# Performance work log

Hardware: AMD Instinct MI355X
Metric: run time of the kernel (lower is better)

Reference implementation:

```python
import jax, jax.numpy as jnp
import numpy as np
from math import log

B, L, D = 2, 4096, 2048
H, Dh, C, KW = 16, 128, 64, 4
EPS = 1e-5
SCALE = 0.02


def setup_inputs() -> dict:
    key = jax.random.key(0)
    ks = jax.random.split(key, 16)
    rn = lambda k, shp, sc=SCALE: jax.random.normal(k, shp, jnp.float32) * sc
    # dt_bias built like the torch module
    dt = jnp.exp(jax.random.uniform(ks[7], (H,)) * (log(0.1) - log(0.001)) + log(0.001))
    dt = jnp.clip(dt, 0.0001, None)
    dt_bias = dt + jnp.log(-jnp.expm1(-dt))
    return {
        "x": jax.random.normal(ks[0], (B, L, D), jnp.float32),
        "Wq": rn(ks[1], (H * Dh, D)),
        "Wk": rn(ks[2], (H * Dh, D)),
        "Wv": rn(ks[3], (H * Dh, D)),
        "Wb": rn(ks[4], (H, D)),
        "Wa": rn(ks[5], (H, D)),
        "A_log": jnp.log(jax.random.uniform(ks[6], (H,), minval=0.01, maxval=16.0)),
        "dt_bias": dt_bias,
        "conv_q": rn(ks[8], (H * Dh, 1, KW), 0.2),
        "conv_k": rn(ks[9], (H * Dh, 1, KW), 0.2),
        "conv_v": rn(ks[10], (H * Dh, 1, KW), 0.2),
        "Wg": rn(ks[11], (H * Dh, D)),
        "norm_w": jnp.ones((Dh,), jnp.float32),
        "Wo": rn(ks[12], (D, H * Dh)),
        "S0": jnp.zeros((B, H, Dh, Dh), jnp.float32),
    }


def _causal_dwconv(x, w):
    # x: [B,L,Ch]; w: [Ch,1,KW] depthwise causal conv (left pad KW-1), then SiLU
    y = jax.lax.conv_general_dilated(
        x.transpose(0, 2, 1), w, (1,), [(KW - 1, 0)],
        feature_group_count=w.shape[0], dimension_numbers=("NCH", "OIH", "NCH"))
    return jax.nn.silu(y).transpose(0, 2, 1)


def reference(x, Wq, Wk, Wv, Wb, Wa, A_log, dt_bias, conv_q, conv_k, conv_v, Wg, norm_w, Wo, S0):
    q = _causal_dwconv(x @ Wq.T, conv_q).reshape(B, L, H, Dh).transpose(0, 2, 1, 3)  # [B,H,L,Dh]
    k = _causal_dwconv(x @ Wk.T, conv_k).reshape(B, L, H, Dh).transpose(0, 2, 1, 3)
    v = _causal_dwconv(x @ Wv.T, conv_v).reshape(B, L, H, Dh).transpose(0, 2, 1, 3)
    beta = jax.nn.sigmoid(x @ Wb.T).transpose(0, 2, 1)                                # [B,H,L]
    g = (-jnp.exp(A_log) * jax.nn.softplus(x @ Wa.T + dt_bias)).transpose(0, 2, 1)    # [B,H,L]
    l2 = lambda t: t / jnp.maximum(jnp.linalg.norm(t, axis=-1, keepdims=True), 1e-12)
    q = l2(q) / (Dh ** 0.5)
    k = l2(k)

    N = L // C  # chunks (L divisible by C)
    chop = lambda t: jnp.moveaxis(t.reshape(B, H, N, C, Dh), 2, 0)   # [N,B,H,C,Dh]
    qc, kc, vc = chop(q), chop(k), chop(v)
    betac = jnp.moveaxis(beta.reshape(B, H, N, C), 2, 0)[..., None]  # [N,B,H,C,1]
    gc = jnp.moveaxis(g.reshape(B, H, N, C), 2, 0)                   # [N,B,H,C]

    eye = jnp.eye(C, dtype=x.dtype)
    m_incl = jnp.tril(jnp.ones((C, C), bool))
    m_strict = jnp.tril(jnp.ones((C, C), bool), -1)

    def step(S, ch):
        Q, Kc, V, bet, gch = ch
        lg = jnp.cumsum(gch, axis=-1)          # log gamma, [B,H,C]
        gamma = jnp.exp(lg)
        lgC = lg[..., -1:]
        gCr = jnp.exp(lgC - lg)
        gammaC = jnp.exp(lgC)[..., None]       # [B,H,1,1]
        Qd = Q * gamma[..., None]
        Kd = gCr[..., None] * Kc
        Sd = S * gammaC
        Gam = lg[..., :, None] - lg[..., None, :]
        ratio = jnp.exp(jnp.where(m_strict, Gam, -jnp.inf))
        A = eye + bet * ratio * (Kc @ jnp.swapaxes(Kc, -1, -2))
        T = jax.scipy.linalg.solve_triangular(A, jnp.broadcast_to(eye, A.shape), lower=True)
        Wm = T @ (bet * gamma[..., None] * Kc)
        U = T @ (bet * V)
        St = jnp.swapaxes(S, -1, -2)
        GM = jnp.exp(jnp.where(m_incl, Gam, -jnp.inf))
        mid = U - Wm @ St                      # [B,H,C,Dh]
        O = Qd @ St + ((Q @ jnp.swapaxes(Kc, -1, -2)) * GM) @ mid
        S_new = Sd + jnp.swapaxes(mid, -1, -2) @ Kd
        return S_new, O

    S_fin, Os = jax.lax.scan(step, S0, (qc, kc, vc, betac, gc))
    o = Os.transpose(1, 0, 3, 2, 4).reshape(B, L, H, Dh)  # chunks -> [B,L,H,Dh]
    gate = (x @ Wg.T).reshape(B, L, H, Dh)
    # gated RMSNorm: rms-normalize o, scale by weight, gate with SiLU(g)
    o = o * jax.lax.rsqrt(jnp.mean(o * o, axis=-1, keepdims=True) + EPS) * norm_w * jax.nn.silu(gate)
    return (o.reshape(B, L, H * Dh) @ Wo.T, S_fin)
```

## Files before the change

kernel.cpp:

```cpp
#include <hip/hip_runtime.h>
#include <math.h>

#define B_   2
#define L_   4096
#define D_   2048
#define H_   16
#define DH   128
#define CH   64
#define NCH  64
#define HD   2048
#define BH   32
#define BHL  131072
#define PSZ  16777216ull

typedef unsigned short u16;
typedef __attribute__((ext_vector_type(8))) short bf16x8;
typedef __attribute__((ext_vector_type(4))) float f32x4;
#define MFMA16(a, b, c) __builtin_amdgcn_mfma_f32_16x16x32_bf16(a, b, c, 0, 0, 0)

static __device__ __forceinline__ float sigm(float x) { return 1.0f / (1.0f + expf(-x)); }

static __device__ __forceinline__ float b2f(u16 u) {
    union { float f; unsigned int i; } v; v.i = ((unsigned int)u) << 16; return v.f;
}
static __device__ __forceinline__ u16 f2b(float f) {
    union { float f; unsigned int i; } v; v.f = f;
    unsigned int r = v.i + 0x7fffu + ((v.i >> 16) & 1u);
    return (u16)(r >> 16);
}
static __device__ __forceinline__ void b8ld(const u16* p, float* d) {
    uint4 u = *(const uint4*)p;
    d[0] = b2f((u16)(u.x & 0xffff)); d[1] = b2f((u16)(u.x >> 16));
    d[2] = b2f((u16)(u.y & 0xffff)); d[3] = b2f((u16)(u.y >> 16));
    d[4] = b2f((u16)(u.z & 0xffff)); d[5] = b2f((u16)(u.z >> 16));
    d[6] = b2f((u16)(u.w & 0xffff)); d[7] = b2f((u16)(u.w >> 16));
}
static __device__ __forceinline__ void b8st(const float* s, u16* p) {
    uint4 u;
    u.x = (unsigned)f2b(s[0]) | ((unsigned)f2b(s[1]) << 16);
    u.y = (unsigned)f2b(s[2]) | ((unsigned)f2b(s[3]) << 16);
    u.z = (unsigned)f2b(s[4]) | ((unsigned)f2b(s[5]) << 16);
    u.w = (unsigned)f2b(s[6]) | ((unsigned)f2b(s[7]) << 16);
    *(uint4*)p = u;
}
static __device__ __forceinline__ void cstore(float* p, float v) { *p = v; }
static __device__ __forceinline__ void cstore(u16* p, float v) { *p = f2b(v); }

static __device__ __forceinline__ void async16(const u16* g, u16* l) {
    __builtin_amdgcn_global_load_lds(
        (const __attribute__((address_space(1))) unsigned int*)g,
        (__attribute__((address_space(3))) unsigned int*)l, 16, 0, 0);
}

static __device__ __forceinline__ void bar_lgkm() {
    asm volatile("s_waitcnt lgkmcnt(0)" ::: "memory");
    __builtin_amdgcn_sched_barrier(0);
    __builtin_amdgcn_s_barrier();
    __builtin_amdgcn_sched_barrier(0);
}
static __device__ __forceinline__ void wait_vm0() {
    asm volatile("s_waitcnt vmcnt(0)" ::: "memory");
    __builtin_amdgcn_sched_barrier(0);
}

__global__ __launch_bounds__(256) void cvt_f2b(const float* __restrict__ in,
                                               u16* __restrict__ out, int n8) {
    int i = blockIdx.x * 256 + threadIdx.x;
    if (i >= n8) return;
    float t[8];
    float4 a = *(const float4*)(in + (size_t)i * 8);
    float4 b = *(const float4*)(in + (size_t)i * 8 + 4);
    t[0] = a.x; t[1] = a.y; t[2] = a.z; t[3] = a.w;
    t[4] = b.x; t[5] = b.y; t[6] = b.z; t[7] = b.w;
    b8st(t, out + (size_t)i * 8);
}

template <typename TC>
__global__ __launch_bounds__(256) void gemm_bt_async(const u16* __restrict__ A,
                                                     const u16* __restrict__ Bm,
                                                     TC* __restrict__ Cm,
                                                     int M, int N, int K) {
    __shared__ __align__(16) u16 sA[128 * 64];
    __shared__ __align__(16) u16 sB[128 * 64];
    const int tid = threadIdx.x;
    const int w = tid >> 6, lane = tid & 63, lq = lane >> 4, ln = lane & 15;
    const int wm = w >> 1, wn = w & 1;
    const int mbase = blockIdx.y * 128, nbase = blockIdx.x * 128;

    f32x4 acc[4][4];
#pragma unroll
    for (int mt = 0; mt < 4; mt++)
#pragma unroll
        for (int nt = 0; nt < 4; nt++) acc[mt][nt] = (f32x4){0.f, 0.f, 0.f, 0.f};

    for (int k0 = 0; k0 < K; k0 += 64) {
#pragma unroll
        for (int j = 0; j < 4; j++) {
            int c = tid + 256 * j;
            int row = c >> 3;
            int oct = (c & 7) ^ (row & 7);
            async16(A + (size_t)(mbase + row) * K + k0 + oct * 8, &sA[c * 8]);
            async16(Bm + (size_t)(nbase + row) * K + k0 + oct * 8, &sB[c * 8]);
        }
        __syncthreads();
#pragma unroll
        for (int ks = 0; ks < 2; ks++) {
            const int o = ks * 4 + lq;
            bf16x8 af[4], bfr[4];
#pragma unroll
            for (int mt = 0; mt < 4; mt++) {
                int m = wm * 64 + mt * 16 + ln;
                af[mt] = *(const bf16x8*)&sA[(m << 6) + ((o ^ (m & 7)) << 3)];
            }
#pragma unroll
            for (int nt = 0; nt < 4; nt++) {
                int nn = wn * 64 + nt * 16 + ln;
                bfr[nt] = *(const bf16x8*)&sB[(nn << 6) + ((o ^ (nn & 7)) << 3)];
            }
#pragma unroll
            for (int mt = 0; mt < 4; mt++)
#pragma unroll
                for (int nt = 0; nt < 4; nt++)
                    acc[mt][nt] = MFMA16(af[mt], bfr[nt], acc[mt][nt]);
        }
        __syncthreads();
    }
#pragma unroll
    for (int mt = 0; mt < 4; mt++)
#pragma unroll
        for (int nt = 0; nt < 4; nt++) {
            int col = nbase + wn * 64 + nt * 16 + ln;
#pragma unroll
            for (int r = 0; r < 4; r++) {
                int row = mbase + wm * 64 + mt * 16 + lq * 4 + r;
                cstore(Cm + (size_t)row * N + col, acc[mt][nt][r]);
            }
        }
}

__global__ __launch_bounds__(256) void conv_silu_norm(const u16* __restrict__ pre,
                                                      const float* __restrict__ w,
                                                      u16* __restrict__ out, int mode) {
    int wid = blockIdx.x * 4 + (threadIdx.x >> 6);
    int lane = threadIdx.x & 63;
    int l = wid & (L_ - 1);
    int bh = wid >> 12;
    int b = bh >> 4, h = bh & 15;

    float vals[2];
    float sumsq = 0.0f;
#pragma unroll
    for (int s = 0; s < 2; s++) {
        int d = lane + 64 * s;
        int c = h * DH + d;
        const u16* col = pre + (size_t)b * L_ * HD + c;
        float acc = 0.0f;
        if (l >= 3) {
            acc = w[c * 4 + 0] * b2f(col[(size_t)(l - 3) * HD]) +
                  w[c * 4 + 1] * b2f(col[(size_t)(l - 2) * HD]) +
                  w[c * 4 + 2] * b2f(col[(size_t)(l - 1) * HD]) +
                  w[c * 4 + 3] * b2f(col[(size_t)l * HD]);
        } else {
#pragma unroll
            for (int j = 0; j < 4; j++) {
                int ll = l - 3 + j;
                if (ll >= 0) acc += w[c * 4 + j] * b2f(col[(size_t)ll * HD]);
            }
        }
        float y = acc * sigm(acc);
        vals[s] = y;
        sumsq += y * y;
    }
    if (mode < 2) {
#pragma unroll
        for (int m = 32; m >= 1; m >>= 1) sumsq += __shfl_xor(sumsq, m, 64);
        float scale = 1.0f / fmaxf(sqrtf(sumsq), 1e-12f);
        if (mode == 0) scale *= 0.08838834764831843f;
        vals[0] *= scale;
        vals[1] *= scale;
    }
    u16* o = out + ((size_t)bh * L_ + l) * DH;
    o[lane] = f2b(vals[0]);
    o[lane + 64] = f2b(vals[1]);
}

__global__ __launch_bounds__(64) void proj_small(const float* __restrict__ x,
                                                 const float* __restrict__ Wb,
                                                 const float* __restrict__ Wa,
                                                 float* __restrict__ bpre,
                                                 float* __restrict__ apre) {
    int row = blockIdx.x;
    int lane = threadIdx.x;
    const float* xr = x + (size_t)row * D_;
    float xv[32];
#pragma unroll
    for (int j = 0; j < 32; j++) xv[j] = xr[lane + 64 * j];
    for (int h = 0; h < 16; h++) {
        const float* wr = Wb + (size_t)h * D_;
        float acc = 0.0f;
#pragma unroll
        for (int j = 0; j < 32; j++) acc += xv[j] * wr[lane + 64 * j];
#pragma unroll
        for (int m = 32; m >= 1; m >>= 1) acc += __shfl_xor(acc, m, 64);
        if (lane == 0) bpre[(size_t)row * 16 + h] = acc;
    }
    for (int h = 0; h < 16; h++) {
        const float* wr = Wa + (size_t)h * D_;
        float acc = 0.0f;
#pragma unroll
        for (int j = 0; j < 32; j++) acc += xv[j] * wr[lane + 64 * j];
#pragma unroll
        for (int m = 32; m >= 1; m >>= 1) acc += __shfl_xor(acc, m, 64);
        if (lane == 0) apre[(size_t)row * 16 + h] = acc;
    }
}

__global__ __launch_bounds__(256) void beta_g_k(const float* __restrict__ bpre,
                                                const float* __restrict__ apre,
                                                const float* __restrict__ A_log,
                                                const float* __restrict__ dt_bias,
                                                float* __restrict__ beta, float* __restrict__ g) {
    int gi = blockIdx.x * 256 + threadIdx.x;
    int l = gi & (L_ - 1);
    int bh = gi >> 12;
    int b = bh >> 4, h = bh & 15;
    float bp = bpre[((size_t)b * L_ + l) * 16 + h];
    float ap = apre[((size_t)b * L_ + l) * 16 + h] + dt_bias[h];
    float sp = (ap > 20.0f) ? ap : log1pf(expf(ap));
    beta[(size_t)bh * L_ + l] = 1.0f / (1.0f + expf(-bp));
    g[(size_t)bh * L_ + l] = -expf(A_log[h]) * sp;
}

__global__ __launch_bounds__(256) void prep_chunks(u16* __restrict__ q, u16* __restrict__ k,
                                                   u16* __restrict__ v,
                                                   const float* __restrict__ beta,
                                                   const float* __restrict__ g,
                                                   u16* __restrict__ Wm, u16* __restrict__ W2,
                                                   float* __restrict__ gamC) {
    __shared__ __align__(16) u16 sKb[64 * 136];
    __shared__ __align__(16) float sA[64 * 65];
    __shared__ __align__(16) float sT[64 * 68];
    __shared__ float sLg[CH], sGam[CH], sGcr[CH], sBeta[CH];

    const int cid = blockIdx.x;
    const int bh = cid >> 6, n = cid & 63;
    const int tid = threadIdx.x;
    const int w = tid >> 6, lane = tid & 63, lq = lane >> 4, ln = lane & 15;
    const size_t cbase = ((size_t)bh * L_ + (size_t)n * CH) * DH;
    u16* qw = q + cbase;
    u16* kw = k + cbase;
    u16* vc = v + cbase;

    bf16x8 aQ[4];
    {
        const u16* qrow = qw + (size_t)(w * 16 + ln) * DH;
#pragma unroll
        for (int ks = 0; ks < 4; ks++)
            aQ[ks] = *(const bf16x8*)(qrow + ks * 32 + lq * 8);
    }
#pragma unroll
    for (int rep = 0; rep < 4; rep++) {
        int f = tid + 256 * rep;
        int row = f >> 4, c8 = (f & 15) * 8;
        *(uint4*)&sKb[row * 136 + c8] = *(const uint4*)(kw + (size_t)row * DH + c8);
    }
    if (tid < 64) {
        float lg = g[(size_t)bh * L_ + (size_t)n * CH + tid];
#pragma unroll
        for (int off = 1; off < 64; off <<= 1) {
            float u = __shfl_up(lg, off, 64);
            if (tid >= off) lg += u;
        }
        float lgC = __shfl(lg, 63, 64);
        sLg[tid] = lg;
        sGam[tid] = expf(lg);
        sGcr[tid] = expf(lgC - lg);
        sBeta[tid] = beta[(size_t)bh * L_ + (size_t)n * CH + tid];
        if (tid == 63) gamC[cid] = expf(lgC);
    }
    __syncthreads();

    {
        f32x4 accA[4], accQ[4];
#pragma unroll
        for (int nt = 0; nt < 4; nt++) {
            accA[nt] = (f32x4){0.f, 0.f, 0.f, 0.f};
            accQ[nt] = (f32x4){0.f, 0.f, 0.f, 0.f};
        }
#pragma unroll
        for (int ks = 0; ks < 4; ks++) {
            int k0 = ks * 32 + lq * 8;
            bf16x8 aK = *(const bf16x8*)&sKb[(w * 16 + ln) * 136 + k0];
#pragma unroll
            for (int nt = 0; nt < 4; nt++) {
                bf16x8 bK = *(const bf16x8*)&sKb[(nt * 16 + ln) * 136 + k0];
                accA[nt] = MFMA16(aK, bK, accA[nt]);
                accQ[nt] = MFMA16(aQ[ks], bK, accQ[nt]);
            }
        }
        for (int idx = tid; idx < 64 * 68; idx += 256) sT[idx] = 0.f;
        u16* w2c = W2 + (size_t)cid * CH * CH;
#pragma unroll
        for (int nt = 0; nt < 4; nt++) {
            int j = nt * 16 + ln;
            float lgj = sLg[j];
#pragma unroll
            for (int r = 0; r < 4; r++) {
                int i = w * 16 + lq * 4 + r;
                float dexp = expf(fminf(sLg[i] - lgj, 0.f));
                sA[i * 65 + j] = (j < i) ? sBeta[i] * dexp * accA[nt][r] : 0.f;
                w2c[i * CH + j] = f2b((j <= i) ? accQ[nt][r] * dexp : 0.f);
            }
        }
    }
    __syncthreads();

    float colv[16];
    {
        const int i0 = w * 16;
        colv[0] = (ln == 0) ? 1.f : 0.f;
#pragma unroll
        for (int i = 1; i < 16; i++) {
            float acc = (ln == i) ? 1.f : 0.f;
#pragma unroll
            for (int kk = 0; kk < 15; kk++) {
                if (kk < i) acc -= sA[(i0 + i) * 65 + i0 + kk] * colv[kk];
            }
            colv[i] = acc;
        }
    }
#pragma unroll
    for (int rep = 0; rep < 4; rep++) {
        int f = tid + 256 * rep;
        int i = f >> 4, d8 = (f & 15) * 8;
        float tq[8];
        b8ld(qw + (size_t)i * DH + d8, tq);
        float sq = sGam[i];
#pragma unroll
        for (int jj = 0; jj < 8; jj++) tq[jj] *= sq;
        b8st(tq, qw + (size_t)i * DH + d8);
    }
    {
        int e = tid >> 1, qh = tid & 1;
#pragma unroll
        for (int oo = 0; oo < 4; oo++) {
            int i0 = qh * 32 + oo * 8;
            u16 op[8];
#pragma unroll
            for (int jj = 0; jj < 8; jj++)
                op[jj] = f2b(b2f(sKb[(i0 + jj) * 136 + e]) * sGcr[i0 + jj]);
            int slot = ((i0 >> 3) ^ (e & 7));
            uint4 pk;
            pk.x = (unsigned)op[0] | ((unsigned)op[1] << 16);
            pk.y = (unsigned)op[2] | ((unsigned)op[3] << 16);
            pk.z = (unsigned)op[4] | ((unsigned)op[5] << 16);
            pk.w = (unsigned)op[6] | ((unsigned)op[7] << 16);
            *(uint4*)(kw + e * 64 + slot * 8) = pk;
        }
    }
    if (lq == 0) {
#pragma unroll
        for (int i = 0; i < 16; i++) sT[(w * 16 + i) * 68 + w * 16 + ln] = colv[i];
    }
    __syncthreads();

    auto trijob = [&](int bi, int bj) {
        float accv[4] = {0.f, 0.f, 0.f, 0.f};
        for (int kb = bj; kb < bi; kb++) {
#pragma unroll
            for (int kk = 0; kk < 16; kk++) {
                float bv = sT[(kb * 16 + kk) * 68 + bj * 16 + ln];
#pragma unroll
                for (int r = 0; r < 4; r++)
                    accv[r] += sA[(bi * 16 + lq * 4 + r) * 65 + kb * 16 + kk] * bv;
            }
        }
        float xv[4] = {0.f, 0.f, 0.f, 0.f};
#pragma unroll
        for (int kk = 0; kk < 16; kk++) {
            float bv = __shfl(accv[kk & 3], (kk >> 2) * 16 + ln, 64);
#pragma unroll
            for (int r = 0; r < 4; r++)
                xv[r] -= sT[(bi * 16 + lq * 4 + r) * 68 + bi * 16 + kk] * bv;
        }
#pragma unroll
        for (int r = 0; r < 4; r++)
            sT[(bi * 16 + lq * 4 + r) * 68 + bj * 16 + ln] = xv[r];
    };
    if (w < 3) trijob(w + 1, w);
    __syncthreads();
    if (w < 2) trijob(w + 2, w);
    __syncthreads();
    if (w == 0) trijob(3, 0);
    __syncthreads();

    {
        int ib = tid >> 4, cb = tid & 15;
        int i0 = ib * 4, c0 = cb * 8;
        float accK[4][8], accV[4][8];
#pragma unroll
        for (int r = 0; r < 4; r++)
#pragma unroll
            for (int c = 0; c < 8; c++) { accK[r][c] = 0.0f; accV[r][c] = 0.0f; }
        for (int kk = 0; kk < CH; kk += 4) {
            float tr[4][4];
#pragma unroll
            for (int r = 0; r < 4; r++) {
                float4 t4 = *(const float4*)&sT[(i0 + r) * 68 + kk];
                tr[r][0] = t4.x; tr[r][1] = t4.y; tr[r][2] = t4.z; tr[r][3] = t4.w;
            }
#pragma unroll
            for (int s = 0; s < 4; s++) {
                int kks = kk + s;
                float va[8], ka[8];
                b8ld(vc + (size_t)kks * DH + c0, va);
                b8ld(&sKb[kks * 136 + c0], ka);
                float bv = sBeta[kks];
                float kf = bv * sGam[kks];
#pragma unroll
                for (int c = 0; c < 8; c++) { va[c] *= bv; ka[c] *= kf; }
#pragma unroll
                for (int r = 0; r < 4; r++) {
                    float t = tr[r][s];
#pragma unroll
                    for (int c = 0; c < 8; c++) {
                        accK[r][c] += t * ka[c];
                        accV[r][c] += t * va[c];
                    }
                }
            }
        }
        u16* wmc = Wm + (size_t)cid * CH * DH;
#pragma unroll
        for (int r = 0; r < 4; r++) b8st(&accK[r][0], wmc + (size_t)(i0 + r) * DH + c0);
        __syncthreads();
#pragma unroll
        for (int r = 0; r < 4; r++) b8st(&accV[r][0], vc + (size_t)(i0 + r) * DH + c0);
    }
}

__global__ __launch_bounds__(256) void scan_mfma(const u16* __restrict__ Wm,
                                                 const u16* __restrict__ U,
                                                 const u16* __restrict__ Qd,
                                                 const u16* __restrict__ Kd,
                                                 const u16* __restrict__ W2,
                                                 const float* __restrict__ gamC,
                                                 const float* __restrict__ S0,
                                                 float* __restrict__ Og,
                                                 float* __restrict__ Sfin) {
    __shared__ __align__(16) u16 sWm[2][64 * 128];
    __shared__ __align__(16) u16 sQd[2][64 * 128];
    __shared__ __align__(16) u16 sW2[2][64 * 64];
    __shared__ __align__(16) u16 sKdT[2][128 * 64];
    __shared__ __align__(16) u16 sS[2][16 * 136];
    __shared__ __align__(16) u16 sMidT[16 * 72];

    const int bid = blockIdx.x;
    const int xcd = bid & 7, slot = bid >> 3;
    const int bh = xcd + 8 * (slot >> 3), dg = slot & 7, d0 = dg * 16;
    const int tid = threadIdx.x;
    const int w = tid >> 6, lane = tid & 63, lq = lane >> 4, ln = lane & 15;

    f32x4 S_t[2];
#pragma unroll
    for (int t2 = 0; t2 < 2; t2++)
#pragma unroll
        for (int r = 0; r < 4; r++)
            S_t[t2][r] = S0[(size_t)bh * DH * DH + (size_t)(d0 + lq * 4 + r) * DH + w * 32 + t2 * 16 + ln];

    auto stage_async = [&](int m, int p) {
        const size_t cid2 = (size_t)bh * NCH + m;
        const u16* wmc = Wm + cid2 * CH * DH;
        const size_t tb = ((size_t)bh * L_ + (size_t)m * CH) * DH;
        const u16* qc  = Qd + tb;
        const u16* kc  = Kd + tb;
        const u16* w2c = W2 + cid2 * CH * CH;
#pragma unroll
        for (int j = 0; j < 4; j++) {
            int c = tid + 256 * j;
            int row = c >> 4;
            int osrc = (c & 15) ^ (row & 7);
            async16(wmc + (size_t)row * DH + osrc * 8, &sWm[p][c * 8]);
            async16(qc  + (size_t)row * DH + osrc * 8, &sQd[p][c * 8]);
            async16(kc + (size_t)c * 8, &sKdT[p][c * 8]);
        }
#pragma unroll
        for (int j = 0; j < 2; j++) {
            int c = tid + 256 * j;
            int row = c >> 3;
            int osrc = (c & 7) ^ (row & 7);
            async16(w2c + (size_t)row * CH + osrc * 8, &sW2[p][c * 8]);
        }
    };
    auto write_ss = [&](int p) {
#pragma unroll
        for (int t2 = 0; t2 < 2; t2++)
#pragma unroll
            for (int r = 0; r < 4; r++)
                sS[p][(lq * 4 + r) * 136 + w * 32 + t2 * 16 + ln] = f2b(S_t[t2][r]);
    };

    u16 ureg[4], uregN[4];
    auto load_ureg = [&](int m, u16* dst) {
        const u16* uc = U + ((size_t)bh * L_ + (size_t)m * CH) * DH;
#pragma unroll
        for (int r = 0; r < 4; r++)
            dst[r] = uc[(size_t)(w * 16 + lq * 4 + r) * DH + d0 + ln];
    };

    stage_async(0, 0);
    load_ureg(0, ureg);
    float gCur = gamC[(size_t)bh * NCH];
    float gNext = 0.f;
    write_ss(0);
    wait_vm0();
    bar_lgkm();

    for (int n = 0; n < NCH; n++) {
        const int p = n & 1;
        const bool hasN = (n + 1 < NCH);
        if (hasN) {
            stage_async(n + 1, p ^ 1);
            load_ureg(n + 1, uregN);
            gNext = gamC[(size_t)bh * NCH + n + 1];
        }

        {
            f32x4 macc = (f32x4){0.f, 0.f, 0.f, 0.f};
            const int i = w * 16 + ln;
#pragma unroll
            for (int ks = 0; ks < 4; ks++) {
                int o = ks * 4 + lq;
                bf16x8 a = *(const bf16x8*)&sWm[p][i * 128 + ((o ^ (i & 7)) << 3)];
                bf16x8 b = *(const bf16x8*)&sS[p][ln * 136 + ks * 32 + lq * 8];
                macc = MFMA16(a, b, macc);
            }
#pragma unroll
            for (int r = 0; r < 4; r++) {
                int ii = w * 16 + lq * 4 + r;
                float mv = b2f(ureg[r]) - macc[r];
                sMidT[ln * 72 + ii] = f2b(mv);
            }
        }
        bar_lgkm();

        {
            f32x4 oacc = (f32x4){0.f, 0.f, 0.f, 0.f};
            const int i = w * 16 + ln;
#pragma unroll
            for (int ks = 0; ks < 4; ks++) {
                int o = ks * 4 + lq;
                bf16x8 a = *(const bf16x8*)&sQd[p][i * 128 + ((o ^ (i & 7)) << 3)];
                bf16x8 b = *(const bf16x8*)&sS[p][ln * 136 + ks * 32 + lq * 8];
                oacc = MFMA16(a, b, oacc);
            }
#pragma unroll
            for (int ks = 0; ks < 2; ks++) {
                int o = ks * 4 + lq;
                bf16x8 a = *(const bf16x8*)&sW2[p][i * 64 + ((o ^ (i & 7)) << 3)];
                bf16x8 b = *(const bf16x8*)&sMidT[ln * 72 + ks * 32 + lq * 8];
                oacc = MFMA16(a, b, oacc);
            }
#pragma unroll
            for (int r = 0; r < 4; r++) {
                int ii = w * 16 + lq * 4 + r;
                Og[((size_t)bh * L_ + (size_t)n * CH + ii) * DH + d0 + ln] = oacc[r];
            }
        }

#pragma unroll
        for (int t2 = 0; t2 < 2; t2++)
#pragma unroll
            for (int r = 0; r < 4; r++) S_t[t2][r] *= gCur;
#pragma unroll
        for (int ks = 0; ks < 2; ks++) {
            bf16x8 a = *(const bf16x8*)&sMidT[ln * 72 + ks * 32 + lq * 8];
#pragma unroll
            for (int t2 = 0; t2 < 2; t2++) {
                int e = (2 * w + t2) * 16 + ln;
                int o = ks * 4 + lq;
                bf16x8 b = *(const bf16x8*)&sKdT[p][e * 64 + ((o ^ (e & 7)) << 3)];
                S_t[t2] = MFMA16(a, b, S_t[t2]);
            }
        }

        if (hasN) {
            write_ss(p ^ 1);
#pragma unroll
            for (int r = 0; r < 4; r++) ureg[r] = uregN[r];
            gCur = gNext;
            wait_vm0();
            bar_lgkm();
        }
    }

#pragma unroll
    for (int t2 = 0; t2 < 2; t2++)
#pragma unroll
        for (int r = 0; r < 4; r++)
            Sfin[(size_t)bh * DH * DH + (size_t)(d0 + lq * 4 + r) * DH + w * 32 + t2 * 16 + ln] = S_t[t2][r];
}

__global__ __launch_bounds__(256) void epilogue_gate(const float* __restrict__ Ob,
                                                     const u16* __restrict__ gpre,
                                                     const float* __restrict__ norm_w,
                                                     u16* __restrict__ gated) {
    int wid = blockIdx.x * 4 + (threadIdx.x >> 6);
    int lane = threadIdx.x & 63;
    int l = wid & (L_ - 1);
    int bh = wid >> 12;
    int b = bh >> 4, h = bh & 15;
    const float* orow = Ob + ((size_t)bh * L_ + l) * DH;
    float o0 = orow[lane], o1 = orow[lane + 64];
    float ss = o0 * o0 + o1 * o1;
#pragma unroll
    for (int m = 32; m >= 1; m >>= 1) ss += __shfl_xor(ss, m, 64);
    float r = rsqrtf(ss * (1.0f / 128.0f) + 1e-5f);
    size_t gidx = ((size_t)b * L_ + l) * HD + h * DH;
    float gp0 = b2f(gpre[gidx + lane]), gp1 = b2f(gpre[gidx + lane + 64]);
    gated[gidx + lane] = f2b(o0 * r * norm_w[lane] * (gp0 * sigm(gp0)));
    gated[gidx + lane + 64] = f2b(o1 * r * norm_w[lane + 64] * (gp1 * sigm(gp1)));
}

extern "C" void kernel_launch(void* const* d_in, const int* in_sizes, int n_in,
                              void* d_out, int out_size, void* d_ws, size_t ws_size,
                              hipStream_t stream) {
    const float* x       = (const float*)d_in[0];
    const float* Wq      = (const float*)d_in[1];
    const float* Wk      = (const float*)d_in[2];
    const float* Wv      = (const float*)d_in[3];
    const float* Wb      = (const float*)d_in[4];
    const float* Wa      = (const float*)d_in[5];
    const float* A_log   = (const float*)d_in[6];
    const float* dt_bias = (const float*)d_in[7];
    const float* conv_q  = (const float*)d_in[8];
    const float* conv_k  = (const float*)d_in[9];
    const float* conv_v  = (const float*)d_in[10];
    const float* Wg      = (const float*)d_in[11];
    const float* norm_w  = (const float*)d_in[12];
    const float* Wo      = (const float*)d_in[13];
    const float* S0      = (const float*)d_in[14];
    float* out = (float*)d_out;

    u16* Pb = (u16*)d_ws;
    u16* Qb = Pb + PSZ;
    u16* Kb = Qb + PSZ;
    u16* Vb = Kb + PSZ;
    u16* W2b = Vb + PSZ;
    u16* xb  = W2b + PSZ / 2;
    u16* wbuf = xb + PSZ;
    float* bpre = (float*)(wbuf + 4194304);
    float* apre = bpre + BHL;
    float* betab = apre + BHL;
    float* gbuf = betab + BHL;
    float* gamC = gbuf + BHL;

    float* Obuf = out;
    float* Sfin = out + PSZ;

    dim3 gblk(16, 64);
    const int W8 = 2048 * 2048 / 8;

    cvt_f2b<<<8192, 256, 0, stream>>>(x, xb, (int)(PSZ / 8));
    cvt_f2b<<<2048, 256, 0, stream>>>(Wq, wbuf, W8);
    gemm_bt_async<u16><<<gblk, 256, 0, stream>>>(xb, wbuf, Pb, 8192, 2048, 2048);
    conv_silu_norm<<<32768, 256, 0, stream>>>(Pb, conv_q, Qb, 0);
    cvt_f2b<<<2048, 256, 0, stream>>>(Wk, wbuf, W8);
    gemm_bt_async<u16><<<gblk, 256, 0, stream>>>(xb, wbuf, Pb, 8192, 2048, 2048);
    conv_silu_norm<<<32768, 256, 0, stream>>>(Pb, conv_k, Kb, 1);
    cvt_f2b<<<2048, 256, 0, stream>>>(Wv, wbuf, W8);
    gemm_bt_async<u16><<<gblk, 256, 0, stream>>>(xb, wbuf, Pb, 8192, 2048, 2048);
    conv_silu_norm<<<32768, 256, 0, stream>>>(Pb, conv_v, Vb, 2);
    proj_small<<<8192, 64, 0, stream>>>(x, Wb, Wa, bpre, apre);
    beta_g_k<<<512, 256, 0, stream>>>(bpre, apre, A_log, dt_bias, betab, gbuf);
    prep_chunks<<<2048, 256, 0, stream>>>(Qb, Kb, Vb, betab, gbuf, Pb, W2b, gamC);
    scan_mfma<<<256, 256, 0, stream>>>(Pb, Vb, Qb, Kb, W2b, gamC, S0, Obuf, Sfin);
    cvt_f2b<<<2048, 256, 0, stream>>>(Wg, wbuf, W8);
    gemm_bt_async<u16><<<gblk, 256, 0, stream>>>(xb, wbuf, Vb, 8192, 2048, 2048);
    epilogue_gate<<<32768, 256, 0, stream>>>(Obuf, Vb, norm_w, Kb);
    cvt_f2b<<<2048, 256, 0, stream>>>(Wo, wbuf, W8);
    gemm_bt_async<float><<<gblk, 256, 0, stream>>>(Kb, wbuf, out, 8192, 2048, 2048);
}
```

Measured before the change: 1.068 ms.

## Use split-bf16 MFMA for T@K and T@V in prep_chunks; swizzle GEMM block order

Replaces the scalar FP32 accumulation of Wm = T·(beta·gamma·K) and U = T·(beta·V) in prep_chunks with bf16 MFMA. T is split into hi and lo bf16 parts to keep accuracy, and K and V are staged transposed with XOR swizzles in reused shared memory. Separately, the GEMM kernel remaps block indices into eight interleaved groups, which is meant to change L2 locality. The split doubles the MFMA count, and the output stores become scalar 2-byte writes instead of vectorized ones.

```diff
diff --git a/kernel.cpp b/kernel.cpp
--- a/kernel.cpp
+++ b/kernel.cpp
@@ -85,7 +85,11 @@
     const int tid = threadIdx.x;
     const int w = tid >> 6, lane = tid & 63, lq = lane >> 4, ln = lane & 15;
     const int wm = w >> 1, wn = w & 1;
-    const int mbase = blockIdx.y * 128, nbase = blockIdx.x * 128;
+    const int nx = gridDim.x;
+    const int lin = blockIdx.y * nx + blockIdx.x;
+    const int chunk = (nx * gridDim.y) >> 3;
+    const int wg = (lin & 7) * chunk + (lin >> 3);
+    const int mbase = (wg / nx) * 128, nbase = (wg % nx) * 128;
 
     f32x4 acc[4][4];
 #pragma unroll
@@ -240,7 +244,12 @@
     __shared__ __align__(16) u16 sKb[64 * 136];
     __shared__ __align__(16) float sA[64 * 65];
     __shared__ __align__(16) float sT[64 * 68];
+    __shared__ __align__(16) u16 sKsT[128 * 64];
     __shared__ float sLg[CH], sGam[CH], sGcr[CH], sBeta[CH];
+
+    u16* sVsT = (u16*)sA;
+    u16* sThi = (u16*)sT;
+    u16* sTlo = (u16*)sT + 4096;
 
     const int cid = blockIdx.x;
     const int bh = cid >> 6, n = cid & 63;
@@ -395,47 +404,133 @@
     __syncthreads();
 
     {
-        int ib = tid >> 4, cb = tid & 15;
-        int i0 = ib * 4, c0 = cb * 8;
-        float accK[4][8], accV[4][8];
-#pragma unroll
-        for (int r = 0; r < 4; r++)
-#pragma unroll
-            for (int c = 0; c < 8; c++) { accK[r][c] = 0.0f; accV[r][c] = 0.0f; }
-        for (int kk = 0; kk < CH; kk += 4) {
-            float tr[4][4];
-#pragma unroll
-            for (int r = 0; r < 4; r++) {
-                float4 t4 = *(const float4*)&sT[(i0 + r) * 68 + kk];
-                tr[r][0] = t4.x; tr[r][1] = t4.y; tr[r][2] = t4.z; tr[r][3] = t4.w;
-            }
-#pragma unroll
-            for (int s = 0; s < 4; s++) {
-                int kks = kk + s;
-                float va[8], ka[8];
-                b8ld(vc + (size_t)kks * DH + c0, va);
-                b8ld(&sKb[kks * 136 + c0], ka);
-                float bv = sBeta[kks];
-                float kf = bv * sGam[kks];
-#pragma unroll
-                for (int c = 0; c < 8; c++) { va[c] *= bv; ka[c] *= kf; }
+        int e = tid >> 1, qh = tid & 1;
+#pragma unroll
+        for (int oo = 0; oo < 4; oo++) {
+            int i0 = qh * 32 + oo * 8;
+            u16 op[8];
+#pragma unroll
+            for (int jj = 0; jj < 8; jj++) {
+                int kkw = i0 + jj;
+                op[jj] = f2b(b2f(sKb[kkw * 136 + e]) * (sBeta[kkw] * sGam[kkw]));
+            }
+            int slot = ((i0 >> 3) ^ (e & 7));
+            uint4 pk;
+            pk.x = (unsigned)op[0] | ((unsigned)op[1] << 16);
+            pk.y = (unsigned)op[2] | ((unsigned)op[3] << 16);
+            pk.z = (unsigned)op[4] | ((unsigned)op[5] << 16);
+            pk.w = (unsigned)op[6] | ((unsigned)op[7] << 16);
+            *(uint4*)&sKsT[e * 64 + slot * 8] = pk;
+        }
+    }
+    float tvs[16];
+    {
+        int ti = tid >> 2, kks = (tid & 3) * 16;
+#pragma unroll
+        for (int j = 0; j < 16; j++) tvs[j] = sT[ti * 68 + kks + j];
+    }
+    __syncthreads();
+
+    {
+        int ti = tid >> 2, kks = (tid & 3) * 16;
+#pragma unroll
+        for (int h = 0; h < 2; h++) {
+            u16 hi8[8], lo8[8];
+#pragma unroll
+            for (int j = 0; j < 8; j++) {
+                float tv = tvs[h * 8 + j];
+                u16 hb = f2b(tv);
+                hi8[j] = hb;
+                lo8[j] = f2b(tv - b2f(hb));
+            }
+            int io = (kks >> 3) + h;
+            int slot = io ^ (ti & 7);
+            uint4 ph, pl;
+            ph.x = (unsigned)hi8[0] | ((unsigned)hi8[1] << 16);
+            ph.y = (unsigned)hi8[2] | ((unsigned)hi8[3] << 16);
+            ph.z = (unsigned)hi8[4] | ((unsigned)hi8[5] << 16);
+            ph.w = (unsigned)hi8[6] | ((unsigned)hi8[7] << 16);
+            pl.x = (unsigned)lo8[0] | ((unsigned)lo8[1] << 16);
+            pl.y = (unsigned)lo8[2] | ((unsigned)lo8[3] << 16);
+            pl.z = (unsigned)lo8[4] | ((unsigned)lo8[5] << 16);
+            pl.w = (unsigned)lo8[6] | ((unsigned)lo8[7] << 16);
+            *(uint4*)&sThi[ti * 64 + slot * 8] = ph;
+            *(uint4*)&sTlo[ti * 64 + slot * 8] = pl;
+        }
+    }
+#pragma unroll
+    for (int rep = 0; rep < 4; rep++) {
+        int f = tid + 256 * rep;
+        int row = f >> 4, c8 = (f & 15) * 8;
+        *(uint4*)&sKb[row * 136 + c8] = *(const uint4*)(vc + (size_t)row * DH + c8);
+    }
+    __syncthreads();
+
+    {
+        int e = tid >> 1, qh = tid & 1;
+#pragma unroll
+        for (int oo = 0; oo < 4; oo++) {
+            int i0 = qh * 32 + oo * 8;
+            u16 op[8];
+#pragma unroll
+            for (int jj = 0; jj < 8; jj++) {
+                int kkw = i0 + jj;
+                op[jj] = f2b(b2f(sKb[kkw * 136 + e]) * sBeta[kkw]);
+            }
+            int slot = ((i0 >> 3) ^ (e & 7));
+            uint4 pk;
+            pk.x = (unsigned)op[0] | ((unsigned)op[1] << 16);
+            pk.y = (unsigned)op[2] | ((unsigned)op[3] << 16);
+            pk.z = (unsigned)op[4] | ((unsigned)op[5] << 16);
+            pk.w = (unsigned)op[6] | ((unsigned)op[7] << 16);
+            *(uint4*)&sVsT[e * 64 + slot * 8] = pk;
+        }
+    }
+    __syncthreads();
+
+    {
+        u16* wmc = Wm + (size_t)cid * CH * DH;
+        bf16x8 bK[2][2], bV[2][2];
+#pragma unroll
+        for (int et = 0; et < 2; et++) {
+            int eb = w * 32 + et * 16 + ln;
+#pragma unroll
+            for (int ks = 0; ks < 2; ks++) {
+                int o = ks * 4 + lq;
+                bK[et][ks] = *(const bf16x8*)&sKsT[eb * 64 + ((o ^ (eb & 7)) << 3)];
+                bV[et][ks] = *(const bf16x8*)&sVsT[eb * 64 + ((o ^ (eb & 7)) << 3)];
+            }
+        }
+#pragma unroll
+        for (int it = 0; it < 4; it++) {
+            int ia = it * 16 + ln;
+            bf16x8 ahi[2], alo[2];
+#pragma unroll
+            for (int ks = 0; ks < 2; ks++) {
+                int o = ks * 4 + lq;
+                ahi[ks] = *(const bf16x8*)&sThi[ia * 64 + ((o ^ (ia & 7)) << 3)];
+                alo[ks] = *(const bf16x8*)&sTlo[ia * 64 + ((o ^ (ia & 7)) << 3)];
+            }
+#pragma unroll
+            for (int et = 0; et < 2; et++) {
+                f32x4 aK = (f32x4){0.f, 0.f, 0.f, 0.f};
+                f32x4 aV = (f32x4){0.f, 0.f, 0.f, 0.f};
+#pragma unroll
+                for (int ks = 0; ks < 2; ks++) {
+                    aK = MFMA16(ahi[ks], bK[et][ks], aK);
+                    aK = MFMA16(alo[ks], bK[et][ks], aK);
+                    aV = MFMA16(ahi[ks], bV[et][ks], aV);
+                    aV = MFMA16(alo[ks], bV[et][ks], aV);
+                }
+                int ecol = w * 32 + et * 16 + ln;
 #pragma unroll
                 for (int r = 0; r < 4; r++) {
-                    float t = tr[r][s];
-#pragma unroll
-                    for (int c = 0; c < 8; c++) {
-                        accK[r][c] += t * ka[c];
-                        accV[r][c] += t * va[c];
-                    }
+                    int irow = it * 16 + lq * 4 + r;
+                    wmc[(size_t)irow * DH + ecol] = f2b(aK[r]);
+                    vc[(size_t)irow * DH + ecol] = f2b(aV[r]);
                 }
             }
         }
-        u16* wmc = Wm + (size_t)cid * CH * DH;
-#pragma unroll
-        for (int r = 0; r < 4; r++) b8st(&accK[r][0], wmc + (size_t)(i0 + r) * DH + c0);
-        __syncthreads();
-#pragma unroll
-        for (int r = 0; r < 4; r++) b8st(&accV[r][0], vc + (size_t)(i0 + r) * DH + c0);
     }
 }
 
```

Result: faster. 1.030 ms (-3.5%).
